# Performance work log

Hardware: AMD Instinct MI355X
Metric: run time of the kernel (lower is better)

## Reference

```python
import jax, jax.numpy as jnp
import numpy as np

EPS = 1e-8  # StyleGAN instance-norm epsilon
LRELU_SLOPE = 0.2


def setup_inputs() -> dict:
    key = jax.random.key(0)
    ks = jax.random.split(key, 8)
    B, H, W, C, NF, ZD = 8, 64, 64, 512, 512, 512
    x = jax.random.normal(ks[0], (B, H, W, C), dtype=jnp.float32)
    dlatents = jax.random.normal(ks[1], (B, ZD), dtype=jnp.float32)
    noise_map = jax.random.normal(ks[2], (B, H, W, 1), dtype=jnp.float32)
    conv_w = jax.random.normal(ks[3], (C, NF), dtype=jnp.float32) * (1.0 / np.sqrt(C))
    noise_weight = jax.random.normal(ks[4], (1, 1, 1, NF), dtype=jnp.float32) * 0.1
    bias = jax.random.normal(ks[5], (1, 1, 1, NF), dtype=jnp.float32) * 0.1
    dense_w = jax.random.normal(ks[6], (ZD, 2 * NF), dtype=jnp.float32) * (1.0 / np.sqrt(ZD))
    dense_b = jax.random.normal(ks[7], (2 * NF,), dtype=jnp.float32) * 0.1
    return {"x": x, "dlatents": dlatents, "noise_map": noise_map, "conv_w": conv_w,
            "noise_weight": noise_weight, "bias": bias, "dense_w": dense_w, "dense_b": dense_b}


def reference(x, dlatents, noise_map, conv_w, noise_weight, bias, dense_w, dense_b):
    # 1x1 conv, no bias: per-pixel GEMM over channels. [B,H,W,C] @ [C,NF]
    y = jnp.einsum('bhwc,cf->bhwf', x, conv_w)
    # spatial noise (per-channel weight) + bias + leaky relu, fused elementwise
    y = jax.nn.leaky_relu(y + noise_weight * noise_map + bias, LRELU_SLOPE)
    # param-free instance norm over spatial dims (per sample, per channel)
    mu = jnp.mean(y, axis=(1, 2), keepdims=True)
    var = jnp.mean(jnp.square(y - mu), axis=(1, 2), keepdims=True)
    yn = (y - mu) * jax.lax.rsqrt(var + EPS)
    # style modulation: dense(dlatents) -> [B, 2, 1, 1, NF] -> gamma, beta
    gb = dlatents @ dense_w + dense_b
    nf = y.shape[-1]
    gb = gb.reshape(-1, 2, 1, 1, nf)
    gamma, beta = gb[:, 0], gb[:, 1]
    return yn * (1.0 + gamma) + beta
```

## Files before the change

kernel.cpp:

```cpp
#include <hip/hip_runtime.h>

typedef unsigned short u16;
typedef unsigned int u32;
typedef __attribute__((ext_vector_type(8))) short short8;
typedef __attribute__((ext_vector_type(4))) float f32x4;
typedef const __attribute__((address_space(1))) void gvoid;
typedef __attribute__((address_space(3))) void lvoid;

#define LRELU_SLOPE 0.2f
#define EPS 1e-8f

static __device__ inline u32 cvt_pk_bf16(float lo, float hi) {
    u32 r;
    asm volatile("v_cvt_pk_bf16_f32 %0, %1, %2" : "=v"(r) : "v"(lo), "v"(hi));
    return r;
}
static __device__ inline u16 f2bf(float x) {
    u32 u = __float_as_uint(x);
    u += 0x7FFF + ((u >> 16) & 1);
    return (u16)(u >> 16);
}

__global__ __launch_bounds__(256) void k_prep(
    const float* __restrict__ w, u16* __restrict__ wts,
    const float* __restrict__ dl, const float* __restrict__ dw,
    const float* __restrict__ db, float* __restrict__ gbuf,
    float* __restrict__ zbase)
{
    __shared__ float sg[256], sb[256];
    const int bx  = blockIdx.x;
    const int tid = threadIdx.x;
    if (bx < 1024) {
        int t = bx * 256 + tid;
        int n = t >> 9, k = t & 511;
        int pos = (k & 448) + ((((k >> 3) ^ n) & 7) << 3) + (k & 7);
        wts[(size_t)n * 512 + pos] = f2bf(w[(size_t)k * 512 + n]);
    } else if (bx < 1152) {
        int idx = bx - 1024;
        int b   = idx >> 4;
        int f   = (idx & 15) * 32 + (tid & 31);
        int kc  = tid >> 5;
        const float* dlb = dl + (size_t)b * 512;
        float g = 0.0f, be = 0.0f;
        #pragma unroll 16
        for (int i = 0; i < 64; ++i) {
            int k = kc * 64 + i;
            float dv = dlb[k];
            g  = fmaf(dv, dw[(size_t)k * 1024 + f], g);
            be = fmaf(dv, dw[(size_t)k * 1024 + 512 + f], be);
        }
        sg[tid] = g; sb[tid] = be;
        __syncthreads();
        if (tid < 32) {
            float gs = db[f], bs = db[512 + f];
            #pragma unroll
            for (int q = 0; q < 8; ++q) { gs += sg[tid + 32 * q]; bs += sb[tid + 32 * q]; }
            gbuf[(size_t)b * 1024 + f]       = gs;
            gbuf[(size_t)b * 1024 + 512 + f] = bs;
        }
    } else {
        float4 z = {0.0f, 0.0f, 0.0f, 0.0f};
        float4* p = (float4*)zbase;
        #pragma unroll
        for (int i = 0; i < 8; ++i)
            p[tid + i * 256] = z;
    }
}

__global__ __launch_bounds__(256, 2) void k_gemm(
    const float* __restrict__ x, const u16* __restrict__ wts,
    const float* __restrict__ noise, const float* __restrict__ nw,
    const float* __restrict__ bias, float* __restrict__ y,
    float* __restrict__ sum, float* __restrict__ sumsq)
{
    __shared__ __align__(16) u16 Al[2][128 * 64];
    __shared__ __align__(16) u16 Bl[2][128 * 64];
    const int tid  = threadIdx.x;
    const int lane = tid & 63;
    const int wid  = tid >> 6;
    const int wm   = wid >> 1, wn = wid & 1;
    const int wg   = blockIdx.x;
    const int swz  = (wg & 7) * 128 + (wg >> 3);
    const int m0   = (swz >> 2) * 128;
    const int n0   = (swz & 3) * 128;

    const int arow = tid >> 3;
    const int acp  = tid & 7;
    const int ac   = acp ^ (arow & 7);
    const float* asrc = x + (size_t)(m0 + arow) * 512 + ac * 8;
    const size_t brow0 = (size_t)(n0 + wid * 32 + (lane >> 3)) * 512 + (lane & 7) * 8;

    f32x4 acc[4][4] = {};
    float4 pa[8];

    #pragma unroll
    for (int j = 0; j < 4; ++j) {
        pa[2 * j]     = *(const float4*)(asrc + (size_t)j * 32 * 512);
        pa[2 * j + 1] = *(const float4*)(asrc + (size_t)j * 32 * 512 + 4);
    }
    #pragma unroll
    for (int i = 0; i < 4; ++i)
        __builtin_amdgcn_global_load_lds((gvoid*)(wts + brow0 + (size_t)i * 8 * 512),
                                         (lvoid*)((char*)Bl[0] + wid * 4096 + i * 1024), 16, 0, 0);
    #pragma unroll
    for (int j = 0; j < 4; ++j) {
        uint4 o;
        o.x = cvt_pk_bf16(pa[2 * j].x, pa[2 * j].y);
        o.y = cvt_pk_bf16(pa[2 * j].z, pa[2 * j].w);
        o.z = cvt_pk_bf16(pa[2 * j + 1].x, pa[2 * j + 1].y);
        o.w = cvt_pk_bf16(pa[2 * j + 1].z, pa[2 * j + 1].w);
        *(uint4*)((char*)Al[0] + (arow + j * 32) * 128 + acp * 16) = o;
    }
    __syncthreads();

    for (int t = 0; t < 8; ++t) {
        const int cb = t & 1, nb = cb ^ 1;
        const int kb = (t + 1) * 64;
        if (t < 7) {
            #pragma unroll
            for (int j = 0; j < 4; ++j) {
                pa[2 * j]     = *(const float4*)(asrc + (size_t)j * 32 * 512 + kb);
                pa[2 * j + 1] = *(const float4*)(asrc + (size_t)j * 32 * 512 + kb + 4);
            }
            #pragma unroll
            for (int i = 0; i < 4; ++i)
                __builtin_amdgcn_global_load_lds((gvoid*)(wts + brow0 + (size_t)i * 8 * 512 + kb),
                                                 (lvoid*)((char*)Bl[nb] + wid * 4096 + i * 1024), 16, 0, 0);
        }
        #pragma unroll
        for (int ks = 0; ks < 2; ++ks) {
            short8 af[4], bf[4];
            const int cidx = ks * 4 + (lane >> 4);
            #pragma unroll
            for (int mi = 0; mi < 4; ++mi) {
                int r = wm * 64 + mi * 16 + (lane & 15);
                af[mi] = *(const short8*)((char*)Al[cb] + r * 128 + ((cidx ^ (r & 7)) * 16));
            }
            #pragma unroll
            for (int ni = 0; ni < 4; ++ni) {
                int r = wn * 64 + ni * 16 + (lane & 15);
                bf[ni] = *(const short8*)((char*)Bl[cb] + r * 128 + ((cidx ^ (r & 7)) * 16));
            }
            #pragma unroll
            for (int mi = 0; mi < 4; ++mi)
                #pragma unroll
                for (int ni = 0; ni < 4; ++ni)
                    acc[mi][ni] = __builtin_amdgcn_mfma_f32_16x16x32_bf16(
                        af[mi], bf[ni], acc[mi][ni], 0, 0, 0);
        }
        if (t < 7) {
            #pragma unroll
            for (int j = 0; j < 4; ++j) {
                uint4 o;
                o.x = cvt_pk_bf16(pa[2 * j].x, pa[2 * j].y);
                o.y = cvt_pk_bf16(pa[2 * j].z, pa[2 * j].w);
                o.z = cvt_pk_bf16(pa[2 * j + 1].x, pa[2 * j + 1].y);
                o.w = cvt_pk_bf16(pa[2 * j + 1].z, pa[2 * j + 1].w);
                *(uint4*)((char*)Al[nb] + (arow + j * 32) * 128 + acp * 16) = o;
            }
            __syncthreads();
        }
    }

    const int b = m0 >> 12;
    float nwv[4], bv[4];
    int colb[4];
    #pragma unroll
    for (int ni = 0; ni < 4; ++ni) {
        int col = n0 + wn * 64 + ni * 16 + (lane & 15);
        colb[ni] = col;
        nwv[ni] = nw[col];
        bv[ni]  = bias[col];
    }
    float ls[4] = {0, 0, 0, 0}, lq[4] = {0, 0, 0, 0};
    #pragma unroll
    for (int mi = 0; mi < 4; ++mi) {
        int rbase = m0 + wm * 64 + mi * 16 + (lane >> 4) * 4;
        #pragma unroll
        for (int r = 0; r < 4; ++r) {
            int row = rbase + r;
            float nz = noise[row];
            #pragma unroll
            for (int ni = 0; ni < 4; ++ni) {
                float v = acc[mi][ni][r] + nwv[ni] * nz + bv[ni];
                v = v > 0.0f ? v : LRELU_SLOPE * v;
                y[(size_t)row * 512 + colb[ni]] = v;
                ls[ni] += v;
                lq[ni] += v * v;
            }
        }
    }
    #pragma unroll
    for (int ni = 0; ni < 4; ++ni) {
        float s = ls[ni], q = lq[ni];
        s += __shfl_xor(s, 16); s += __shfl_xor(s, 32);
        q += __shfl_xor(q, 16); q += __shfl_xor(q, 32);
        if ((lane >> 4) == 0) {
            atomicAdd(&sum[b * 512 + colb[ni]], s);
            atomicAdd(&sumsq[b * 512 + colb[ni]], q);
        }
    }
}

__global__ __launch_bounds__(256) void k_norm(
    float* __restrict__ y, const float* __restrict__ sum, const float* __restrict__ sumsq,
    const float* __restrict__ gbuf)
{
    size_t i8 = (size_t)(blockIdx.x * 256 + threadIdx.x) * 8;
    int row = (int)(i8 >> 9);
    int f0  = (int)(i8 & 511);
    int b   = row >> 12;
    int t   = b * 512 + f0;
    float s[8], q[8], g[8], be[8];
    *(float4*)(s)      = *(const float4*)(sum + t);
    *(float4*)(s + 4)  = *(const float4*)(sum + t + 4);
    *(float4*)(q)      = *(const float4*)(sumsq + t);
    *(float4*)(q + 4)  = *(const float4*)(sumsq + t + 4);
    *(float4*)(g)      = *(const float4*)(gbuf + b * 1024 + f0);
    *(float4*)(g + 4)  = *(const float4*)(gbuf + b * 1024 + f0 + 4);
    *(float4*)(be)     = *(const float4*)(gbuf + b * 1024 + 512 + f0);
    *(float4*)(be + 4) = *(const float4*)(gbuf + b * 1024 + 512 + f0 + 4);
    float v[8];
    *(float4*)(v)     = *(float4*)(y + i8);
    *(float4*)(v + 4) = *(float4*)(y + i8 + 4);
    #pragma unroll
    for (int i = 0; i < 8; ++i) {
        float mu  = s[i] * (1.0f / 4096.0f);
        float var = q[i] * (1.0f / 4096.0f) - mu * mu;
        float A   = rsqrtf(var + EPS) * (1.0f + g[i]);
        float C   = be[i] - mu * A;
        v[i] = v[i] * A + C;
    }
    *(float4*)(y + i8)     = *(float4*)(v);
    *(float4*)(y + i8 + 4) = *(float4*)(v + 4);
}

extern "C" void kernel_launch(void* const* d_in, const int* in_sizes, int n_in,
                              void* d_out, int out_size, void* d_ws, size_t ws_size,
                              hipStream_t stream) {
    const float* x     = (const float*)d_in[0];
    const float* dl    = (const float*)d_in[1];
    const float* noise = (const float*)d_in[2];
    const float* w     = (const float*)d_in[3];
    const float* nw    = (const float*)d_in[4];
    const float* bias  = (const float*)d_in[5];
    const float* dw    = (const float*)d_in[6];
    const float* db    = (const float*)d_in[7];
    float* out = (float*)d_out;

    char* ws = (char*)d_ws;
    u16*   wts   = (u16*)ws;
    float* sum   = (float*)(ws + 524288);
    float* sumsq = (float*)(ws + 540672);
    float* gbuf  = (float*)(ws + 557056);

    k_prep<<<1153, 256, 0, stream>>>(w, wts, dl, dw, db, gbuf, sum);
    k_gemm<<<1024, 256, 0, stream>>>(x, wts, noise, nw, bias, out, sum, sumsq);
    k_norm<<<8192, 256, 0, stream>>>(out, sum, sumsq, gbuf);
}
```

Measured before the change: 179.2 us.

## Fuse GEMM and instance norm via persistent grid barrier, full-N tiles

Merges the GEMM and the normalization kernels into one persistent kernel of 256 blocks with 512 threads. Each block computes a 128x512 output tile held in registers, contributes its column sums, waits on a global atomic counter barrier, and then applies the norm and style affine before writing the output once. This removes the write and reread of the intermediate y tensor and one kernel launch. A operands are now loaded straight from global into registers as MFMA fragments instead of being staged through LDS, and the weights are re-laid out for direct fragment loads. The spin barrier requires all 256 blocks to be co-resident, and the large accumulator set raises register pressure.

```diff
diff --git a/kernel.cpp b/kernel.cpp
--- a/kernel.cpp
+++ b/kernel.cpp
@@ -9,6 +9,7 @@
 
 #define LRELU_SLOPE 0.2f
 #define EPS 1e-8f
+#define NBLK 256u
 
 static __device__ inline u32 cvt_pk_bf16(float lo, float hi) {
     u32 r;
@@ -25,7 +26,7 @@
     const float* __restrict__ w, u16* __restrict__ wts,
     const float* __restrict__ dl, const float* __restrict__ dw,
     const float* __restrict__ db, float* __restrict__ gbuf,
-    float* __restrict__ zbase)
+    float* __restrict__ zbase, u32* __restrict__ ctr)
 {
     __shared__ float sg[256], sb[256];
     const int bx  = blockIdx.x;
@@ -33,8 +34,8 @@
     if (bx < 1024) {
         int t = bx * 256 + tid;
         int n = t >> 9, k = t & 511;
-        int pos = (k & 448) + ((((k >> 3) ^ n) & 7) << 3) + (k & 7);
-        wts[(size_t)n * 512 + pos] = f2bf(w[(size_t)k * 512 + n]);
+        int kbb = k >> 5, c = (k >> 3) & 3, ke = k & 7;
+        wts[(size_t)kbb * 16384 + c * 4096 + n * 8 + ke] = f2bf(w[(size_t)k * 512 + n]);
     } else if (bx < 1152) {
         int idx = bx - 1024;
         int b   = idx >> 4;
@@ -64,175 +65,156 @@
         #pragma unroll
         for (int i = 0; i < 8; ++i)
             p[tid + i * 256] = z;
-    }
-}
-
-__global__ __launch_bounds__(256, 2) void k_gemm(
+        if (tid == 0) *ctr = 0u;
+    }
+}
+
+__global__ __launch_bounds__(512, 2) void k_fused(
     const float* __restrict__ x, const u16* __restrict__ wts,
     const float* __restrict__ noise, const float* __restrict__ nw,
-    const float* __restrict__ bias, float* __restrict__ y,
-    float* __restrict__ sum, float* __restrict__ sumsq)
+    const float* __restrict__ bias, const float* __restrict__ gbuf,
+    float* __restrict__ sum, float* __restrict__ sumsq,
+    u32* __restrict__ ctr, float* __restrict__ out)
 {
-    __shared__ __align__(16) u16 Al[2][128 * 64];
-    __shared__ __align__(16) u16 Bl[2][128 * 64];
+    __shared__ __align__(16) u16 Bl[2][16384];
     const int tid  = threadIdx.x;
     const int lane = tid & 63;
     const int wid  = tid >> 6;
-    const int wm   = wid >> 1, wn = wid & 1;
+    const int wm   = wid >> 2;
+    const int wn   = wid & 3;
+    const int lr   = lane & 15;
+    const int lc   = lane >> 4;
     const int wg   = blockIdx.x;
-    const int swz  = (wg & 7) * 128 + (wg >> 3);
-    const int m0   = (swz >> 2) * 128;
-    const int n0   = (swz & 3) * 128;
-
-    const int arow = tid >> 3;
-    const int acp  = tid & 7;
-    const int ac   = acp ^ (arow & 7);
-    const float* asrc = x + (size_t)(m0 + arow) * 512 + ac * 8;
-    const size_t brow0 = (size_t)(n0 + wid * 32 + (lane >> 3)) * 512 + (lane & 7) * 8;
-
-    f32x4 acc[4][4] = {};
-    float4 pa[8];
-
-    #pragma unroll
-    for (int j = 0; j < 4; ++j) {
-        pa[2 * j]     = *(const float4*)(asrc + (size_t)j * 32 * 512);
-        pa[2 * j + 1] = *(const float4*)(asrc + (size_t)j * 32 * 512 + 4);
+    const int swz  = (wg & 7) * 32 + (wg >> 3);
+    const int m0   = swz * 128;
+
+    const float* asrc = x + (size_t)(m0 + wm * 64 + lr) * 512 + lc * 8;
+    const u16* bsrc = wts + (size_t)(wid * 4) * 512 + (size_t)lane * 8;
+    char* bdst = (char*)&Bl[0][0];
+
+    f32x4  acc[4][8] = {};
+    float4 pa[2][8];
+
+    #pragma unroll
+    for (int mi = 0; mi < 4; ++mi) {
+        pa[0][2 * mi]     = *(const float4*)(asrc + (size_t)mi * 16 * 512);
+        pa[0][2 * mi + 1] = *(const float4*)(asrc + (size_t)mi * 16 * 512 + 4);
     }
     #pragma unroll
     for (int i = 0; i < 4; ++i)
-        __builtin_amdgcn_global_load_lds((gvoid*)(wts + brow0 + (size_t)i * 8 * 512),
-                                         (lvoid*)((char*)Bl[0] + wid * 4096 + i * 1024), 16, 0, 0);
-    #pragma unroll
-    for (int j = 0; j < 4; ++j) {
-        uint4 o;
-        o.x = cvt_pk_bf16(pa[2 * j].x, pa[2 * j].y);
-        o.y = cvt_pk_bf16(pa[2 * j].z, pa[2 * j].w);
-        o.z = cvt_pk_bf16(pa[2 * j + 1].x, pa[2 * j + 1].y);
-        o.w = cvt_pk_bf16(pa[2 * j + 1].z, pa[2 * j + 1].w);
-        *(uint4*)((char*)Al[0] + (arow + j * 32) * 128 + acp * 16) = o;
-    }
+        __builtin_amdgcn_global_load_lds((gvoid*)(bsrc + (size_t)i * 512),
+                                         (lvoid*)(bdst + (wid * 4 + i) * 1024), 16, 0, 0);
     __syncthreads();
 
-    for (int t = 0; t < 8; ++t) {
+    #pragma unroll
+    for (int t = 0; t < 16; ++t) {
         const int cb = t & 1, nb = cb ^ 1;
-        const int kb = (t + 1) * 64;
-        if (t < 7) {
-            #pragma unroll
-            for (int j = 0; j < 4; ++j) {
-                pa[2 * j]     = *(const float4*)(asrc + (size_t)j * 32 * 512 + kb);
-                pa[2 * j + 1] = *(const float4*)(asrc + (size_t)j * 32 * 512 + kb + 4);
+        short8 af[4];
+        #pragma unroll
+        for (int mi = 0; mi < 4; ++mi) {
+            union { u32 u[4]; short8 s; } fa;
+            float4 v0 = pa[cb][2 * mi], v1 = pa[cb][2 * mi + 1];
+            fa.u[0] = cvt_pk_bf16(v0.x, v0.y);
+            fa.u[1] = cvt_pk_bf16(v0.z, v0.w);
+            fa.u[2] = cvt_pk_bf16(v1.x, v1.y);
+            fa.u[3] = cvt_pk_bf16(v1.z, v1.w);
+            af[mi] = fa.s;
+        }
+        if (t < 15) {
+            const int kb = (t + 1) * 32;
+            #pragma unroll
+            for (int mi = 0; mi < 4; ++mi) {
+                pa[nb][2 * mi]     = *(const float4*)(asrc + (size_t)mi * 16 * 512 + kb);
+                pa[nb][2 * mi + 1] = *(const float4*)(asrc + (size_t)mi * 16 * 512 + kb + 4);
             }
             #pragma unroll
             for (int i = 0; i < 4; ++i)
-                __builtin_amdgcn_global_load_lds((gvoid*)(wts + brow0 + (size_t)i * 8 * 512 + kb),
-                                                 (lvoid*)((char*)Bl[nb] + wid * 4096 + i * 1024), 16, 0, 0);
-        }
-        #pragma unroll
-        for (int ks = 0; ks < 2; ++ks) {
-            short8 af[4], bf[4];
-            const int cidx = ks * 4 + (lane >> 4);
-            #pragma unroll
-            for (int mi = 0; mi < 4; ++mi) {
-                int r = wm * 64 + mi * 16 + (lane & 15);
-                af[mi] = *(const short8*)((char*)Al[cb] + r * 128 + ((cidx ^ (r & 7)) * 16));
-            }
-            #pragma unroll
-            for (int ni = 0; ni < 4; ++ni) {
-                int r = wn * 64 + ni * 16 + (lane & 15);
-                bf[ni] = *(const short8*)((char*)Bl[cb] + r * 128 + ((cidx ^ (r & 7)) * 16));
-            }
+                __builtin_amdgcn_global_load_lds(
+                    (gvoid*)(bsrc + (size_t)(t + 1) * 16384 + (size_t)i * 512),
+                    (lvoid*)(bdst + nb * 32768 + (wid * 4 + i) * 1024), 16, 0, 0);
+        }
+        #pragma unroll
+        for (int ni = 0; ni < 8; ++ni) {
+            short8 bf = *(const short8*)(bdst + cb * 32768 + lc * 8192 +
+                                         (wn * 128 + ni * 16 + lr) * 16);
             #pragma unroll
             for (int mi = 0; mi < 4; ++mi)
-                #pragma unroll
-                for (int ni = 0; ni < 4; ++ni)
-                    acc[mi][ni] = __builtin_amdgcn_mfma_f32_16x16x32_bf16(
-                        af[mi], bf[ni], acc[mi][ni], 0, 0, 0);
-        }
-        if (t < 7) {
-            #pragma unroll
-            for (int j = 0; j < 4; ++j) {
-                uint4 o;
-                o.x = cvt_pk_bf16(pa[2 * j].x, pa[2 * j].y);
-                o.y = cvt_pk_bf16(pa[2 * j].z, pa[2 * j].w);
-                o.z = cvt_pk_bf16(pa[2 * j + 1].x, pa[2 * j + 1].y);
-                o.w = cvt_pk_bf16(pa[2 * j + 1].z, pa[2 * j + 1].w);
-                *(uint4*)((char*)Al[nb] + (arow + j * 32) * 128 + acp * 16) = o;
-            }
-            __syncthreads();
-        }
+                acc[mi][ni] = __builtin_amdgcn_mfma_f32_16x16x32_bf16(
+                    af[mi], bf, acc[mi][ni], 0, 0, 0);
+        }
+        __syncthreads();
     }
 
     const int b = m0 >> 12;
-    float nwv[4], bv[4];
-    int colb[4];
-    #pragma unroll
-    for (int ni = 0; ni < 4; ++ni) {
-        int col = n0 + wn * 64 + ni * 16 + (lane & 15);
-        colb[ni] = col;
+    float nwv[8], bv[8];
+    #pragma unroll
+    for (int ni = 0; ni < 8; ++ni) {
+        int col = wn * 128 + ni * 16 + lr;
         nwv[ni] = nw[col];
         bv[ni]  = bias[col];
     }
-    float ls[4] = {0, 0, 0, 0}, lq[4] = {0, 0, 0, 0};
+    float ls[8] = {}, lq[8] = {};
     #pragma unroll
     for (int mi = 0; mi < 4; ++mi) {
-        int rbase = m0 + wm * 64 + mi * 16 + (lane >> 4) * 4;
         #pragma unroll
         for (int r = 0; r < 4; ++r) {
-            int row = rbase + r;
+            int row = m0 + wm * 64 + mi * 16 + lc * 4 + r;
             float nz = noise[row];
             #pragma unroll
-            for (int ni = 0; ni < 4; ++ni) {
+            for (int ni = 0; ni < 8; ++ni) {
                 float v = acc[mi][ni][r] + nwv[ni] * nz + bv[ni];
                 v = v > 0.0f ? v : LRELU_SLOPE * v;
-                y[(size_t)row * 512 + colb[ni]] = v;
+                acc[mi][ni][r] = v;
                 ls[ni] += v;
                 lq[ni] += v * v;
             }
         }
     }
     #pragma unroll
-    for (int ni = 0; ni < 4; ++ni) {
+    for (int ni = 0; ni < 8; ++ni) {
         float s = ls[ni], q = lq[ni];
         s += __shfl_xor(s, 16); s += __shfl_xor(s, 32);
         q += __shfl_xor(q, 16); q += __shfl_xor(q, 32);
-        if ((lane >> 4) == 0) {
-            atomicAdd(&sum[b * 512 + colb[ni]], s);
-            atomicAdd(&sumsq[b * 512 + colb[ni]], q);
-        }
-    }
-}
-
-__global__ __launch_bounds__(256) void k_norm(
-    float* __restrict__ y, const float* __restrict__ sum, const float* __restrict__ sumsq,
-    const float* __restrict__ gbuf)
-{
-    size_t i8 = (size_t)(blockIdx.x * 256 + threadIdx.x) * 8;
-    int row = (int)(i8 >> 9);
-    int f0  = (int)(i8 & 511);
-    int b   = row >> 12;
-    int t   = b * 512 + f0;
-    float s[8], q[8], g[8], be[8];
-    *(float4*)(s)      = *(const float4*)(sum + t);
-    *(float4*)(s + 4)  = *(const float4*)(sum + t + 4);
-    *(float4*)(q)      = *(const float4*)(sumsq + t);
-    *(float4*)(q + 4)  = *(const float4*)(sumsq + t + 4);
-    *(float4*)(g)      = *(const float4*)(gbuf + b * 1024 + f0);
-    *(float4*)(g + 4)  = *(const float4*)(gbuf + b * 1024 + f0 + 4);
-    *(float4*)(be)     = *(const float4*)(gbuf + b * 1024 + 512 + f0);
-    *(float4*)(be + 4) = *(const float4*)(gbuf + b * 1024 + 512 + f0 + 4);
-    float v[8];
-    *(float4*)(v)     = *(float4*)(y + i8);
-    *(float4*)(v + 4) = *(float4*)(y + i8 + 4);
-    #pragma unroll
-    for (int i = 0; i < 8; ++i) {
-        float mu  = s[i] * (1.0f / 4096.0f);
-        float var = q[i] * (1.0f / 4096.0f) - mu * mu;
-        float A   = rsqrtf(var + EPS) * (1.0f + g[i]);
-        float C   = be[i] - mu * A;
-        v[i] = v[i] * A + C;
-    }
-    *(float4*)(y + i8)     = *(float4*)(v);
-    *(float4*)(y + i8 + 4) = *(float4*)(v + 4);
+        if (lane < 16) {
+            int col = wn * 128 + ni * 16 + lr;
+            atomicAdd(&sum[b * 512 + col], s);
+            atomicAdd(&sumsq[b * 512 + col], q);
+        }
+    }
+
+    __threadfence();
+    __syncthreads();
+    if (tid == 0) {
+        atomicAdd(ctr, 1u);
+        while (__hip_atomic_load(ctr, __ATOMIC_ACQUIRE, __HIP_MEMORY_SCOPE_AGENT) < NBLK)
+            __builtin_amdgcn_s_sleep(8);
+    }
+    __syncthreads();
+
+    float Af[8], Cf[8];
+    #pragma unroll
+    for (int ni = 0; ni < 8; ++ni) {
+        int col = wn * 128 + ni * 16 + lr;
+        float s = __hip_atomic_load(&sum[b * 512 + col],   __ATOMIC_RELAXED, __HIP_MEMORY_SCOPE_AGENT);
+        float q = __hip_atomic_load(&sumsq[b * 512 + col], __ATOMIC_RELAXED, __HIP_MEMORY_SCOPE_AGENT);
+        float g  = gbuf[b * 1024 + col];
+        float be = gbuf[b * 1024 + 512 + col];
+        float mu  = s * (1.0f / 4096.0f);
+        float var = q * (1.0f / 4096.0f) - mu * mu;
+        float A = rsqrtf(var + EPS) * (1.0f + g);
+        Af[ni] = A;
+        Cf[ni] = be - mu * A;
+    }
+    #pragma unroll
+    for (int mi = 0; mi < 4; ++mi) {
+        #pragma unroll
+        for (int r = 0; r < 4; ++r) {
+            size_t ro = (size_t)(m0 + wm * 64 + mi * 16 + lc * 4 + r) * 512;
+            #pragma unroll
+            for (int ni = 0; ni < 8; ++ni)
+                out[ro + wn * 128 + ni * 16 + lr] = acc[mi][ni][r] * Af[ni] + Cf[ni];
+        }
+    }
 }
 
 extern "C" void kernel_launch(void* const* d_in, const int* in_sizes, int n_in,
@@ -253,8 +235,8 @@
     float* sum   = (float*)(ws + 524288);
     float* sumsq = (float*)(ws + 540672);
     float* gbuf  = (float*)(ws + 557056);
-
-    k_prep<<<1153, 256, 0, stream>>>(w, wts, dl, dw, db, gbuf, sum);
-    k_gemm<<<1024, 256, 0, stream>>>(x, wts, noise, nw, bias, out, sum, sumsq);
-    k_norm<<<8192, 256, 0, stream>>>(out, sum, sumsq, gbuf);
-}
+    u32*   ctr   = (u32*)(ws + 589824);
+
+    k_prep <<<1153, 256, 0, stream>>>(w, wts, dl, dw, db, gbuf, sum, ctr);
+    k_fused<<<256, 512, 0, stream>>>(x, wts, noise, nw, bias, gbuf, sum, sumsq, ctr, out);
+}
```

New measurement: 242.4 us. 1.35x slower.
